# Kernel tuning notes

Hardware: AMD Instinct MI355X
Metric: run time of the kernel (lower is better)

Reference implementation:

```python
import jax, jax.numpy as jnp
import numpy as np

# Brevitas-style per-tensor affine (symmetric) quantization:
#   scale = max|x| / qmax  (stats-derived, treated as constant)
#   q     = clamp(round(x/scale), qmin, qmax) * scale

def _quant_pt(x, bits):
    qmax = 2.0 ** (bits - 1) - 1.0
    qmin = -(2.0 ** (bits - 1))
    scale = jax.lax.stop_gradient(jnp.max(jnp.abs(x))) / qmax
    scale = jnp.maximum(scale, jnp.asarray(1e-8, x.dtype))
    q = jnp.clip(jnp.round(x / scale), qmin, qmax)
    return q * scale, scale


def setup_inputs() -> dict:
    key = jax.random.key(0)
    k1, k2, k3 = jax.random.split(key, 3)
    in_features, out_features, tokens = 4096, 4096, 8192
    inp = jax.random.normal(k1, (tokens, in_features), dtype=jnp.float32)
    # Kaiming-ish init for linear weight [out, in]
    W = jax.random.normal(k2, (out_features, in_features), dtype=jnp.float32) / np.sqrt(in_features)
    b = jax.random.normal(k3, (out_features,), dtype=jnp.float32) * 0.01
    return {"inp": inp, "W": W, "b": b}


def reference(inp, W, b):
    # input quant: Int8 act per-tensor (QuantIdentity default)
    x_dq, s_in = _quant_pt(inp, 8)
    # weight quant: 4-bit per-tensor
    w_dq, s_w = _quant_pt(W, 4)
    # bias quant: Int32 with scale = s_in * s_w
    s_b = s_in * s_w
    b_dq = jnp.round(b / s_b) * s_b  # int32 range never clips realistic biases
    # matmul in dequantized domain (numerically equal to int GEMM * s_in*s_w)
    y = jnp.einsum('ti,oi->to', x_dq, w_dq) + b_dq
    # output quant: Int8 act per-tensor
    y_dq, _ = _quant_pt(y, 8)
    return y_dq
```

## Files before the change

kernel.cpp:

```cpp
#include <hip/hip_runtime.h>


typedef int v4i __attribute__((ext_vector_type(4)));

#define AS1(p) ((const __attribute__((address_space(1))) void*)(p))
#define AS3(p) ((__attribute__((address_space(3))) void*)(p))

#define GM 8192
#define GN 4096
#define GK 4096
#define NBN 16
#define NWG 512

__global__ __launch_bounds__(256) void maxabs_kernel(const float* __restrict__ x, int n4,
                                                     unsigned* __restrict__ slot) {
  __shared__ float red[4];
  int tid = blockIdx.x * blockDim.x + threadIdx.x;
  int stride = gridDim.x * blockDim.x;
  float m = 0.0f;
  const float4* x4 = (const float4*)x;
  for (int i = tid; i < n4; i += stride) {
    float4 v = x4[i];
    m = fmaxf(m, fmaxf(fmaxf(fabsf(v.x), fabsf(v.y)), fmaxf(fabsf(v.z), fabsf(v.w))));
  }
  for (int off = 32; off; off >>= 1) m = fmaxf(m, __shfl_xor(m, off));
  if ((threadIdx.x & 63) == 0) red[threadIdx.x >> 6] = m;
  __syncthreads();
  if (threadIdx.x == 0) {
    float b = fmaxf(fmaxf(red[0], red[1]), fmaxf(red[2], red[3]));
    atomicMax(slot, __float_as_uint(b));
  }
}

__global__ __launch_bounds__(256) void quant_kernel(const float* __restrict__ x,
                                                    signed char* __restrict__ q, int n4,
                                                    const unsigned* __restrict__ slot,
                                                    float qmaxv, float qlo, float qhi) {
  float s = fmaxf(__uint_as_float(*slot) / qmaxv, 1e-8f);
  float inv = 1.0f / s;
  int tid = blockIdx.x * blockDim.x + threadIdx.x;
  int stride = gridDim.x * blockDim.x;
  const float4* x4 = (const float4*)x;
  int* q4 = (int*)q;
  for (int i = tid; i < n4; i += stride) {
    float4 v = x4[i];
    int a0 = (int)fminf(fmaxf(rintf(v.x * inv), qlo), qhi);
    int a1 = (int)fminf(fmaxf(rintf(v.y * inv), qlo), qhi);
    int a2 = (int)fminf(fmaxf(rintf(v.z * inv), qlo), qhi);
    int a3 = (int)fminf(fmaxf(rintf(v.w * inv), qlo), qhi);
    q4[i] = (a0 & 255) | ((a1 & 255) << 8) | ((a2 & 255) << 16) | ((a3 & 255) << 24);
  }
}

__global__ __launch_bounds__(512, 2) void gemm_i8_kernel(const signed char* __restrict__ Xq,
                                                         const signed char* __restrict__ Wq,
                                                         const float* __restrict__ bias,
                                                         const unsigned* __restrict__ slots,
                                                         float* __restrict__ Y,
                                                         unsigned* __restrict__ maxY) {
  __shared__ signed char smem[131072];
  const int tid = threadIdx.x;
  const int wid = tid >> 6, lane = tid & 63;
  const int wr = wid >> 2, wc = wid & 3;
  const int lr = lane & 15, lg = lane >> 4;

  const int bid = (int)blockIdx.x;
  const int swz = (bid & 7) * (NWG / 8) + (bid >> 3);
  const int brow = (swz / NBN) * 256;
  const int bcol = (swz % NBN) * 256;

  const int srr = tid >> 3;
  const int sgl = (tid & 7) ^ (srr & 7);

  int aoff[4], asw[4], boff[4], bsw[4];
#pragma unroll
  for (int mm = 0; mm < 4; ++mm) {
    int hr = wr * 64 + mm * 16 + lr;
    aoff[mm] = hr * 128;
    asw[mm] = hr & 7;
  }
#pragma unroll
  for (int nn = 0; nn < 4; ++nn) {
    int hr = wc * 32 + (nn & 1) * 16 + lr;
    boff[nn] = hr * 128;
    bsw[nn] = hr & 7;
  }

#define ASLOT(db, h) (smem + ((db) * 2 + (h)) * 16384)
#define BSLOT(db, h) (smem + 65536 + ((db) * 2 + (h)) * 16384)
#define STAGE(gptr, grow0, kofs, slot)                                                        \
  {                                                                                           \
    const signed char* _s0 = (gptr) + (size_t)((grow0) + srr) * GK + (kofs) + sgl * 16;       \
    __builtin_amdgcn_global_load_lds(AS1(_s0), AS3((slot) + wid * 1024), 16, 0, 0);           \
    __builtin_amdgcn_global_load_lds(AS1(_s0 + (size_t)64 * GK),                              \
                                     AS3((slot) + 8192 + wid * 1024), 16, 0, 0);              \
  }
#define LDA(mm, db, h, kk) \
  *(const v4i*)(ASLOT(db, h) + aoff[mm] + ((((kk)*4 + lg) ^ asw[mm]) << 4))
#define LDB(nn, db, kk) \
  *(const v4i*)(BSLOT(db, (nn) >> 1) + boff[nn] + ((((kk)*4 + lg) ^ bsw[nn]) << 4))
#define MFMA16(arow)                                                                          \
  __builtin_amdgcn_s_setprio(1);                                                              \
  _Pragma("unroll") for (int mm = 0; mm < 4; ++mm)                                            \
      _Pragma("unroll") for (int nn = 0; nn < 4; ++nn)                                        \
          acc[(arow) + mm][nn] =                                                              \
      __builtin_amdgcn_mfma_i32_16x16x64_i8(af[mm], bf[nn], acc[(arow) + mm][nn], 0, 0, 0);   \
  __builtin_amdgcn_s_setprio(0);

  STAGE(Wq, bcol, 0, BSLOT(0, 0));
  STAGE(Wq, bcol + 128, 0, BSLOT(0, 1));
  STAGE(Xq, brow, 0, ASLOT(0, 0));
  STAGE(Xq, brow + 128, 0, ASLOT(0, 1));

  v4i acc[8][4] = {};

#pragma unroll 2
  for (int t = 0; t < 32; ++t) {
    const int db = t & 1, ndb = db ^ 1;
    const int kof = (t + 1) * 128;
    v4i af[4], bf[4];

    if (t < 31) STAGE(Wq, bcol, kof, BSLOT(ndb, 0));
    if (t == 31)
      asm volatile("s_waitcnt vmcnt(0)" ::: "memory");
    else
      asm volatile("s_waitcnt vmcnt(2)" ::: "memory");
    __builtin_amdgcn_s_barrier();

#pragma unroll
    for (int mm = 0; mm < 4; ++mm) af[mm] = LDA(mm, db, 0, 0);
#pragma unroll
    for (int nn = 0; nn < 4; ++nn) bf[nn] = LDB(nn, db, 0);
    if (t < 31) STAGE(Wq, bcol + 128, kof, BSLOT(ndb, 1));
    asm volatile("s_waitcnt lgkmcnt(0)");
    MFMA16(0)
    __builtin_amdgcn_s_barrier();

#pragma unroll
    for (int mm = 0; mm < 4; ++mm) af[mm] = LDA(mm, db, 1, 0);
    if (t < 31) STAGE(Xq, brow, kof, ASLOT(ndb, 0));
    asm volatile("s_waitcnt lgkmcnt(0)");
    MFMA16(4)
    __builtin_amdgcn_s_barrier();

#pragma unroll
    for (int mm = 0; mm < 4; ++mm) af[mm] = LDA(mm, db, 0, 1);
#pragma unroll
    for (int nn = 0; nn < 4; ++nn) bf[nn] = LDB(nn, db, 1);
    if (t < 31) STAGE(Xq, brow + 128, kof, ASLOT(ndb, 1));
    asm volatile("s_waitcnt lgkmcnt(0)");
    MFMA16(0)
    __builtin_amdgcn_s_barrier();

#pragma unroll
    for (int mm = 0; mm < 4; ++mm) af[mm] = LDA(mm, db, 1, 1);
    asm volatile("s_waitcnt lgkmcnt(0)");
    MFMA16(4)
    __builtin_amdgcn_s_barrier();
  }

  float s_in = fmaxf(__uint_as_float(slots[0]) / 127.0f, 1e-8f);
  float s_w = fmaxf(__uint_as_float(slots[1]) / 7.0f, 1e-8f);
  float s_b = s_in * s_w;
  float lmax = 0.0f;
#pragma unroll
  for (int n = 0; n < 4; ++n) {
    int o = bcol + (n >> 1) * 128 + wc * 32 + (n & 1) * 16 + lr;
    float bdq = rintf(bias[o] / s_b) * s_b;
#pragma unroll
    for (int m = 0; m < 8; ++m) {
      int t0 = brow + (m >> 2) * 128 + wr * 64 + (m & 3) * 16 + (lg << 2);
#pragma unroll
      for (int r2 = 0; r2 < 4; ++r2) {
        float yv = (float)acc[m][n][r2] * s_b + bdq;
        Y[(size_t)(t0 + r2) * GN + o] = yv;
        lmax = fmaxf(lmax, fabsf(yv));
      }
    }
  }
  for (int off = 32; off; off >>= 1) lmax = fmaxf(lmax, __shfl_xor(lmax, off));
  float* fred = (float*)smem;
  if (lane == 0) fred[wid] = lmax;
  __syncthreads();
  if (tid == 0) {
    float m = fred[0];
#pragma unroll
    for (int i = 1; i < 8; ++i) m = fmaxf(m, fred[i]);
    atomicMax(maxY, __float_as_uint(m));
  }
#undef STAGE
#undef ASLOT
#undef BSLOT
#undef LDA
#undef LDB
#undef MFMA16
}

__global__ __launch_bounds__(256) void quant_out_kernel(float* __restrict__ y, int n4,
                                                        const unsigned* __restrict__ slot) {
  float s = fmaxf(__uint_as_float(*slot) / 127.0f, 1e-8f);
  float inv = 1.0f / s;
  int tid = blockIdx.x * blockDim.x + threadIdx.x;
  int stride = gridDim.x * blockDim.x;
  float4* y4 = (float4*)y;
  for (int i = tid; i < n4; i += stride) {
    float4 v = y4[i];
    v.x = fminf(fmaxf(rintf(v.x * inv), -128.0f), 127.0f) * s;
    v.y = fminf(fmaxf(rintf(v.y * inv), -128.0f), 127.0f) * s;
    v.z = fminf(fmaxf(rintf(v.z * inv), -128.0f), 127.0f) * s;
    v.w = fminf(fmaxf(rintf(v.w * inv), -128.0f), 127.0f) * s;
    y4[i] = v;
  }
}

extern "C" void kernel_launch(void* const* d_in, const int* in_sizes, int n_in,
                              void* d_out, int out_size, void* d_ws, size_t ws_size,
                              hipStream_t stream) {
  const float* inp = (const float*)d_in[0];
  const float* W = (const float*)d_in[1];
  const float* b = (const float*)d_in[2];
  float* out = (float*)d_out;

  unsigned* slots = (unsigned*)d_ws;
  signed char* Xq = (signed char*)d_ws + 256;
  signed char* Wq = Xq + (size_t)GM * GK;

  const int nX = GM * GK;
  const int nW = GN * GK;

  hipMemsetAsync(d_ws, 0, 16, stream);

  maxabs_kernel<<<1024, 256, 0, stream>>>(inp, nX / 4, slots + 0);
  maxabs_kernel<<<512, 256, 0, stream>>>(W, nW / 4, slots + 1);

  quant_kernel<<<1024, 256, 0, stream>>>(inp, Xq, nX / 4, slots + 0, 127.0f, -128.0f, 127.0f);
  quant_kernel<<<512, 256, 0, stream>>>(W, Wq, nW / 4, slots + 1, 7.0f, -8.0f, 7.0f);

  gemm_i8_kernel<<<NWG, 512, 0, stream>>>(Xq, Wq, b, slots, out, slots + 2);

  quant_out_kernel<<<1024, 256, 0, stream>>>(out, (GM * GN) / 4, slots + 2);
}
```

Baseline: 265.9 us.

## Restructure GEMM main loop to one barrier per K-step with register double-buffered fragments

Replaces the four-phase K-step, which had a barrier after each MFMA group and staggered global loads, with a single wait-and-barrier at the top of each iteration. All four next-tile global-to-LDS loads are then issued at once, and LDS fragment reads are double-buffered in registers so they overlap the MFMA groups. The aim is to cut barrier and synchronisation stalls. In exchange it raises register pressure, and the full vmcnt(0) wait at the top of each iteration may expose global load latency.

```diff
diff --git a/kernel.cpp b/kernel.cpp
--- a/kernel.cpp
+++ b/kernel.cpp
@@ -99,12 +99,12 @@
   *(const v4i*)(ASLOT(db, h) + aoff[mm] + ((((kk)*4 + lg) ^ asw[mm]) << 4))
 #define LDB(nn, db, kk) \
   *(const v4i*)(BSLOT(db, (nn) >> 1) + boff[nn] + ((((kk)*4 + lg) ^ bsw[nn]) << 4))
-#define MFMA16(arow)                                                                          \
+#define MFMA16(arow, AF, BF)                                                                  \
   __builtin_amdgcn_s_setprio(1);                                                              \
   _Pragma("unroll") for (int mm = 0; mm < 4; ++mm)                                            \
       _Pragma("unroll") for (int nn = 0; nn < 4; ++nn)                                        \
           acc[(arow) + mm][nn] =                                                              \
-      __builtin_amdgcn_mfma_i32_16x16x64_i8(af[mm], bf[nn], acc[(arow) + mm][nn], 0, 0, 0);   \
+      __builtin_amdgcn_mfma_i32_16x16x64_i8(AF[mm], BF[nn], acc[(arow) + mm][nn], 0, 0, 0);   \
   __builtin_amdgcn_s_setprio(0);
 
   STAGE(Wq, bcol, 0, BSLOT(0, 0));
@@ -118,45 +118,36 @@
   for (int t = 0; t < 32; ++t) {
     const int db = t & 1, ndb = db ^ 1;
     const int kof = (t + 1) * 128;
-    v4i af[4], bf[4];
-
-    if (t < 31) STAGE(Wq, bcol, kof, BSLOT(ndb, 0));
-    if (t == 31)
-      asm volatile("s_waitcnt vmcnt(0)" ::: "memory");
-    else
-      asm volatile("s_waitcnt vmcnt(2)" ::: "memory");
+
+    asm volatile("s_waitcnt lgkmcnt(0)" ::: "memory");
+    asm volatile("s_waitcnt vmcnt(0)" ::: "memory");
     __builtin_amdgcn_s_barrier();
-
-#pragma unroll
-    for (int mm = 0; mm < 4; ++mm) af[mm] = LDA(mm, db, 0, 0);
-#pragma unroll
-    for (int nn = 0; nn < 4; ++nn) bf[nn] = LDB(nn, db, 0);
-    if (t < 31) STAGE(Wq, bcol + 128, kof, BSLOT(ndb, 1));
-    asm volatile("s_waitcnt lgkmcnt(0)");
-    MFMA16(0)
-    __builtin_amdgcn_s_barrier();
-
-#pragma unroll
-    for (int mm = 0; mm < 4; ++mm) af[mm] = LDA(mm, db, 1, 0);
-    if (t < 31) STAGE(Xq, brow, kof, ASLOT(ndb, 0));
-    asm volatile("s_waitcnt lgkmcnt(0)");
-    MFMA16(4)
-    __builtin_amdgcn_s_barrier();
-
-#pragma unroll
-    for (int mm = 0; mm < 4; ++mm) af[mm] = LDA(mm, db, 0, 1);
-#pragma unroll
-    for (int nn = 0; nn < 4; ++nn) bf[nn] = LDB(nn, db, 1);
-    if (t < 31) STAGE(Xq, brow + 128, kof, ASLOT(ndb, 1));
-    asm volatile("s_waitcnt lgkmcnt(0)");
-    MFMA16(0)
-    __builtin_amdgcn_s_barrier();
-
-#pragma unroll
-    for (int mm = 0; mm < 4; ++mm) af[mm] = LDA(mm, db, 1, 1);
-    asm volatile("s_waitcnt lgkmcnt(0)");
-    MFMA16(4)
-    __builtin_amdgcn_s_barrier();
+    asm volatile("" ::: "memory");
+
+    if (t < 31) {
+      STAGE(Wq, bcol, kof, BSLOT(ndb, 0));
+      STAGE(Wq, bcol + 128, kof, BSLOT(ndb, 1));
+      STAGE(Xq, brow, kof, ASLOT(ndb, 0));
+      STAGE(Xq, brow + 128, kof, ASLOT(ndb, 1));
+    }
+
+    v4i af0[4], af1[4], bf0[4], bf1[4];
+#pragma unroll
+    for (int mm = 0; mm < 4; ++mm) af0[mm] = LDA(mm, db, 0, 0);
+#pragma unroll
+    for (int nn = 0; nn < 4; ++nn) bf0[nn] = LDB(nn, db, 0);
+#pragma unroll
+    for (int mm = 0; mm < 4; ++mm) af1[mm] = LDA(mm, db, 1, 0);
+    MFMA16(0, af0, bf0)
+#pragma unroll
+    for (int mm = 0; mm < 4; ++mm) af0[mm] = LDA(mm, db, 0, 1);
+#pragma unroll
+    for (int nn = 0; nn < 4; ++nn) bf1[nn] = LDB(nn, db, 1);
+    MFMA16(4, af1, bf0)
+#pragma unroll
+    for (int mm = 0; mm < 4; ++mm) af1[mm] = LDA(mm, db, 1, 1);
+    MFMA16(0, af0, bf1)
+    MFMA16(4, af1, bf1)
   }
 
   float s_in = fmaxf(__uint_as_float(slots[0]) / 127.0f, 1e-8f);
```

After: 368.5 us. 1.39x slower.

## Double-buffer MFMA register fragments to overlap LDS reads with MFMAs

Applied to the files above, without the earlier changes.

Splits the A and B fragment registers into two sets so the next sub-step's LDS reads are issued before the current MFMA block runs. The manual lgkmcnt(0) waits are dropped, leaving the compiler to place finer-grained waits. The trailing barrier of each k-iteration is removed. This aims to hide LDS latency behind matrix math and cut sync stalls, at the cost of more VGPRs and a tighter LDS reuse ordering that depends on the remaining barriers.

```diff
diff --git a/kernel.cpp b/kernel.cpp
--- a/kernel.cpp
+++ b/kernel.cpp
@@ -99,13 +99,16 @@
   *(const v4i*)(ASLOT(db, h) + aoff[mm] + ((((kk)*4 + lg) ^ asw[mm]) << 4))
 #define LDB(nn, db, kk) \
   *(const v4i*)(BSLOT(db, (nn) >> 1) + boff[nn] + ((((kk)*4 + lg) ^ bsw[nn]) << 4))
-#define MFMA16(arow)                                                                          \
+#define MFMA16(arow, AF, BF)                                                                  \
   __builtin_amdgcn_s_setprio(1);                                                              \
   _Pragma("unroll") for (int mm = 0; mm < 4; ++mm)                                            \
       _Pragma("unroll") for (int nn = 0; nn < 4; ++nn)                                        \
           acc[(arow) + mm][nn] =                                                              \
-      __builtin_amdgcn_mfma_i32_16x16x64_i8(af[mm], bf[nn], acc[(arow) + mm][nn], 0, 0, 0);   \
+      __builtin_amdgcn_mfma_i32_16x16x64_i8(AF[mm], BF[nn], acc[(arow) + mm][nn], 0, 0, 0);   \
   __builtin_amdgcn_s_setprio(0);
+#define BAR()                         \
+  __builtin_amdgcn_s_barrier();       \
+  asm volatile("" ::: "memory");
 
   STAGE(Wq, bcol, 0, BSLOT(0, 0));
   STAGE(Wq, bcol + 128, 0, BSLOT(0, 1));
@@ -118,45 +121,41 @@
   for (int t = 0; t < 32; ++t) {
     const int db = t & 1, ndb = db ^ 1;
     const int kof = (t + 1) * 128;
-    v4i af[4], bf[4];
+    v4i af_a[4], af_b[4], bf_a[4], bf_b[4];
 
     if (t < 31) STAGE(Wq, bcol, kof, BSLOT(ndb, 0));
     if (t == 31)
       asm volatile("s_waitcnt vmcnt(0)" ::: "memory");
     else
       asm volatile("s_waitcnt vmcnt(2)" ::: "memory");
-    __builtin_amdgcn_s_barrier();
-
-#pragma unroll
-    for (int mm = 0; mm < 4; ++mm) af[mm] = LDA(mm, db, 0, 0);
-#pragma unroll
-    for (int nn = 0; nn < 4; ++nn) bf[nn] = LDB(nn, db, 0);
+    BAR()
+
+#pragma unroll
+    for (int mm = 0; mm < 4; ++mm) af_a[mm] = LDA(mm, db, 0, 0);
+#pragma unroll
+    for (int nn = 0; nn < 4; ++nn) bf_a[nn] = LDB(nn, db, 0);
+
+#pragma unroll
+    for (int mm = 0; mm < 4; ++mm) af_b[mm] = LDA(mm, db, 1, 0);
     if (t < 31) STAGE(Wq, bcol + 128, kof, BSLOT(ndb, 1));
-    asm volatile("s_waitcnt lgkmcnt(0)");
-    MFMA16(0)
-    __builtin_amdgcn_s_barrier();
-
-#pragma unroll
-    for (int mm = 0; mm < 4; ++mm) af[mm] = LDA(mm, db, 1, 0);
+    MFMA16(0, af_a, bf_a)
+    BAR()
+
+#pragma unroll
+    for (int mm = 0; mm < 4; ++mm) af_a[mm] = LDA(mm, db, 0, 1);
+#pragma unroll
+    for (int nn = 0; nn < 4; ++nn) bf_b[nn] = LDB(nn, db, 1);
     if (t < 31) STAGE(Xq, brow, kof, ASLOT(ndb, 0));
-    asm volatile("s_waitcnt lgkmcnt(0)");
-    MFMA16(4)
-    __builtin_amdgcn_s_barrier();
-
-#pragma unroll
-    for (int mm = 0; mm < 4; ++mm) af[mm] = LDA(mm, db, 0, 1);
-#pragma unroll
-    for (int nn = 0; nn < 4; ++nn) bf[nn] = LDB(nn, db, 1);
+    MFMA16(4, af_b, bf_a)
+    BAR()
+
+#pragma unroll
+    for (int mm = 0; mm < 4; ++mm) af_b[mm] = LDA(mm, db, 1, 1);
     if (t < 31) STAGE(Xq, brow + 128, kof, ASLOT(ndb, 1));
-    asm volatile("s_waitcnt lgkmcnt(0)");
-    MFMA16(0)
-    __builtin_amdgcn_s_barrier();
-
-#pragma unroll
-    for (int mm = 0; mm < 4; ++mm) af[mm] = LDA(mm, db, 1, 1);
-    asm volatile("s_waitcnt lgkmcnt(0)");
-    MFMA16(4)
-    __builtin_amdgcn_s_barrier();
+    MFMA16(0, af_a, bf_b)
+    BAR()
+
+    MFMA16(4, af_b, bf_b)
   }
 
   float s_in = fmaxf(__uint_as_float(slots[0]) / 127.0f, 1e-8f);
@@ -194,6 +193,7 @@
 #undef LDA
 #undef LDB
 #undef MFMA16
+#undef BAR
 }
 
 __global__ __launch_bounds__(256) void quant_out_kernel(float* __restrict__ y, int n4,
```

Measured after the change: 393.3 us. +47.9%, slower.

## Shrink int8 GEMM tile to 128x128 with 4 waves and 2048 workgroups

Applied to the files above, without the earlier changes.

Replaces the 256x256-tile, 8-wave, 128KB-LDS GEMM with a 128x128-tile, 4-wave, 64KB-LDS layout launched over 2048 workgroups. The pipeline goes from four sub-phases per K step to two, and each stage now waits for all outstanding loads (vmcnt(0)) before the barrier. The goal is better occupancy and load balance across CUs. The cost is lower arithmetic intensity per tile, more global traffic, and weaker overlap of loads with MFMA work.

```diff
diff --git a/kernel.cpp b/kernel.cpp
--- a/kernel.cpp
+++ b/kernel.cpp
@@ -9,8 +9,7 @@
 #define GM 8192
 #define GN 4096
 #define GK 4096
-#define NBN 16
-#define NWG 512
+#define NWG 2048
 
 __global__ __launch_bounds__(256) void maxabs_kernel(const float* __restrict__ x, int n4,
                                                      unsigned* __restrict__ slot) {
@@ -52,25 +51,22 @@
   }
 }
 
-__global__ __launch_bounds__(512, 2) void gemm_i8_kernel(const signed char* __restrict__ Xq,
+__global__ __launch_bounds__(256, 2) void gemm_i8_kernel(const signed char* __restrict__ Xq,
                                                          const signed char* __restrict__ Wq,
                                                          const float* __restrict__ bias,
                                                          const unsigned* __restrict__ slots,
                                                          float* __restrict__ Y,
                                                          unsigned* __restrict__ maxY) {
-  __shared__ signed char smem[131072];
+  __shared__ signed char smem[65536];
   const int tid = threadIdx.x;
   const int wid = tid >> 6, lane = tid & 63;
-  const int wr = wid >> 2, wc = wid & 3;
+  const int wr = wid >> 1, wc = wid & 1;
   const int lr = lane & 15, lg = lane >> 4;
 
   const int bid = (int)blockIdx.x;
   const int swz = (bid & 7) * (NWG / 8) + (bid >> 3);
-  const int brow = (swz / NBN) * 256;
-  const int bcol = (swz % NBN) * 256;
-
-  const int srr = tid >> 3;
-  const int sgl = (tid & 7) ^ (srr & 7);
+  const int brow = (swz >> 5) * 128;
+  const int bcol = (swz & 31) * 128;
 
   int aoff[4], asw[4], boff[4], bsw[4];
 #pragma unroll
@@ -81,38 +77,38 @@
   }
 #pragma unroll
   for (int nn = 0; nn < 4; ++nn) {
-    int hr = wc * 32 + (nn & 1) * 16 + lr;
+    int hr = wc * 64 + nn * 16 + lr;
     boff[nn] = hr * 128;
     bsw[nn] = hr & 7;
   }
 
-#define ASLOT(db, h) (smem + ((db) * 2 + (h)) * 16384)
-#define BSLOT(db, h) (smem + 65536 + ((db) * 2 + (h)) * 16384)
+#define ASLOT(db) (smem + (db) * 16384)
+#define BSLOT(db) (smem + 32768 + (db) * 16384)
 #define STAGE(gptr, grow0, kofs, slot)                                                        \
   {                                                                                           \
-    const signed char* _s0 = (gptr) + (size_t)((grow0) + srr) * GK + (kofs) + sgl * 16;       \
-    __builtin_amdgcn_global_load_lds(AS1(_s0), AS3((slot) + wid * 1024), 16, 0, 0);           \
-    __builtin_amdgcn_global_load_lds(AS1(_s0 + (size_t)64 * GK),                              \
-                                     AS3((slot) + 8192 + wid * 1024), 16, 0, 0);              \
-  }
-#define LDA(mm, db, h, kk) \
-  *(const v4i*)(ASLOT(db, h) + aoff[mm] + ((((kk)*4 + lg) ^ asw[mm]) << 4))
+    _Pragma("unroll") for (int _j = 0; _j < 4; ++_j) {                                        \
+      int _r = _j * 32 + wid * 8 + (lane >> 3);                                               \
+      int _g = (lane & 7) ^ (_r & 7);                                                         \
+      const signed char* _s = (gptr) + (size_t)((grow0) + _r) * GK + (kofs) + _g * 16;        \
+      __builtin_amdgcn_global_load_lds(AS1(_s), AS3((slot) + _j * 4096 + wid * 1024), 16, 0,  \
+                                       0);                                                    \
+    }                                                                                         \
+  }
+#define LDA(mm, db, kk) \
+  *(const v4i*)(ASLOT(db) + aoff[mm] + ((((kk)*4 + lg) ^ asw[mm]) << 4))
 #define LDB(nn, db, kk) \
-  *(const v4i*)(BSLOT(db, (nn) >> 1) + boff[nn] + ((((kk)*4 + lg) ^ bsw[nn]) << 4))
-#define MFMA16(arow)                                                                          \
+  *(const v4i*)(BSLOT(db) + boff[nn] + ((((kk)*4 + lg) ^ bsw[nn]) << 4))
+#define MFMA16()                                                                              \
   __builtin_amdgcn_s_setprio(1);                                                              \
   _Pragma("unroll") for (int mm = 0; mm < 4; ++mm)                                            \
-      _Pragma("unroll") for (int nn = 0; nn < 4; ++nn)                                        \
-          acc[(arow) + mm][nn] =                                                              \
-      __builtin_amdgcn_mfma_i32_16x16x64_i8(af[mm], bf[nn], acc[(arow) + mm][nn], 0, 0, 0);   \
+      _Pragma("unroll") for (int nn = 0; nn < 4; ++nn) acc[mm][nn] =                          \
+      __builtin_amdgcn_mfma_i32_16x16x64_i8(af[mm], bf[nn], acc[mm][nn], 0, 0, 0);            \
   __builtin_amdgcn_s_setprio(0);
 
-  STAGE(Wq, bcol, 0, BSLOT(0, 0));
-  STAGE(Wq, bcol + 128, 0, BSLOT(0, 1));
-  STAGE(Xq, brow, 0, ASLOT(0, 0));
-  STAGE(Xq, brow + 128, 0, ASLOT(0, 1));
-
-  v4i acc[8][4] = {};
+  STAGE(Xq, brow, 0, ASLOT(0));
+  STAGE(Wq, bcol, 0, BSLOT(0));
+
+  v4i acc[4][4] = {};
 
 #pragma unroll 2
   for (int t = 0; t < 32; ++t) {
@@ -120,43 +116,29 @@
     const int kof = (t + 1) * 128;
     v4i af[4], bf[4];
 
-    if (t < 31) STAGE(Wq, bcol, kof, BSLOT(ndb, 0));
-    if (t == 31)
-      asm volatile("s_waitcnt vmcnt(0)" ::: "memory");
-    else
-      asm volatile("s_waitcnt vmcnt(2)" ::: "memory");
+    asm volatile("s_waitcnt vmcnt(0)" ::: "memory");
     __builtin_amdgcn_s_barrier();
-
-#pragma unroll
-    for (int mm = 0; mm < 4; ++mm) af[mm] = LDA(mm, db, 0, 0);
+    asm volatile("" ::: "memory");
+
+#pragma unroll
+    for (int mm = 0; mm < 4; ++mm) af[mm] = LDA(mm, db, 0);
 #pragma unroll
     for (int nn = 0; nn < 4; ++nn) bf[nn] = LDB(nn, db, 0);
-    if (t < 31) STAGE(Wq, bcol + 128, kof, BSLOT(ndb, 1));
+    if (t < 31) STAGE(Xq, brow, kof, ASLOT(ndb));
     asm volatile("s_waitcnt lgkmcnt(0)");
-    MFMA16(0)
+    MFMA16()
     __builtin_amdgcn_s_barrier();
-
-#pragma unroll
-    for (int mm = 0; mm < 4; ++mm) af[mm] = LDA(mm, db, 1, 0);
-    if (t < 31) STAGE(Xq, brow, kof, ASLOT(ndb, 0));
+    asm volatile("" ::: "memory");
+
+#pragma unroll
+    for (int mm = 0; mm < 4; ++mm) af[mm] = LDA(mm, db, 1);
+#pragma unroll
+    for (int nn = 0; nn < 4; ++nn) bf[nn] = LDB(nn, db, 1);
+    if (t < 31) STAGE(Wq, bcol, kof, BSLOT(ndb));
     asm volatile("s_waitcnt lgkmcnt(0)");
-    MFMA16(4)
+    MFMA16()
     __builtin_amdgcn_s_barrier();
-
-#pragma unroll
-    for (int mm = 0; mm < 4; ++mm) af[mm] = LDA(mm, db, 0, 1);
-#pragma unroll
-    for (int nn = 0; nn < 4; ++nn) bf[nn] = LDB(nn, db, 1);
-    if (t < 31) STAGE(Xq, brow + 128, kof, ASLOT(ndb, 1));
-    asm volatile("s_waitcnt lgkmcnt(0)");
-    MFMA16(0)
-    __builtin_amdgcn_s_barrier();
-
-#pragma unroll
-    for (int mm = 0; mm < 4; ++mm) af[mm] = LDA(mm, db, 1, 1);
-    asm volatile("s_waitcnt lgkmcnt(0)");
-    MFMA16(4)
-    __builtin_amdgcn_s_barrier();
+    asm volatile("" ::: "memory");
   }
 
   float s_in = fmaxf(__uint_as_float(slots[0]) / 127.0f, 1e-8f);
@@ -165,11 +147,11 @@
   float lmax = 0.0f;
 #pragma unroll
   for (int n = 0; n < 4; ++n) {
-    int o = bcol + (n >> 1) * 128 + wc * 32 + (n & 1) * 16 + lr;
+    int o = bcol + wc * 64 + n * 16 + lr;
     float bdq = rintf(bias[o] / s_b) * s_b;
 #pragma unroll
-    for (int m = 0; m < 8; ++m) {
-      int t0 = brow + (m >> 2) * 128 + wr * 64 + (m & 3) * 16 + (lg << 2);
+    for (int m = 0; m < 4; ++m) {
+      int t0 = brow + wr * 64 + m * 16 + (lg << 2);
 #pragma unroll
       for (int r2 = 0; r2 < 4; ++r2) {
         float yv = (float)acc[m][n][r2] * s_b + bdq;
@@ -180,12 +162,11 @@
   }
   for (int off = 32; off; off >>= 1) lmax = fmaxf(lmax, __shfl_xor(lmax, off));
   float* fred = (float*)smem;
+  __syncthreads();
   if (lane == 0) fred[wid] = lmax;
   __syncthreads();
   if (tid == 0) {
-    float m = fred[0];
-#pragma unroll
-    for (int i = 1; i < 8; ++i) m = fmaxf(m, fred[i]);
+    float m = fmaxf(fmaxf(fred[0], fred[1]), fmaxf(fred[2], fred[3]));
     atomicMax(maxY, __float_as_uint(m));
   }
 #undef STAGE
@@ -236,7 +217,7 @@
   quant_kernel<<<1024, 256, 0, stream>>>(inp, Xq, nX / 4, slots + 0, 127.0f, -128.0f, 127.0f);
   quant_kernel<<<512, 256, 0, stream>>>(W, Wq, nW / 4, slots + 1, 7.0f, -8.0f, 7.0f);
 
-  gemm_i8_kernel<<<NWG, 512, 0, stream>>>(Xq, Wq, b, slots, out, slots + 2);
+  gemm_i8_kernel<<<NWG, 256, 0, stream>>>(Xq, Wq, b, slots, out, slots + 2);
 
   quant_out_kernel<<<1024, 256, 0, stream>>>(out, (GM * GN) / 4, slots + 2);
 }
```

Result: slower. 303.3 us (+14.1%).
